# Kernel tuning notes

Measured on AMD Instinct MI355X. Metric: run time of the kernel, lower is better.

Reference implementation:

```python
import jax, jax.numpy as jnp
import numpy as np

B, H, W, C, NH, WS, SS = 32, 56, 56, 192, 6, 7, 3
N = WS * WS
HD = C // NH
NW = (H // WS) * (W // WS)
HID = 4 * C
RPB_SIZE = (2 * WS - 1) * (2 * WS - 1)


def _rel_index():
    coords = np.stack(np.meshgrid(np.arange(WS), np.arange(WS), indexing='ij')).reshape(2, -1)
    rel = (coords[:, :, None] - coords[:, None, :]).transpose(1, 2, 0)
    rel[..., 0] += WS - 1
    rel[..., 1] += WS - 1
    rel[..., 0] *= 2 * WS - 1
    return rel.sum(-1)  # (N, N) int

REL_IDX = jnp.asarray(_rel_index())


def _swin_attn_mask():
    # standard Swin shifted-window mask: -100 for cross-region pairs
    img = np.zeros((H, W))
    cnt = 0
    for hs in (slice(0, -WS), slice(-WS, -SS), slice(-SS, None)):
        for ws_ in (slice(0, -WS), slice(-WS, -SS), slice(-SS, None)):
            img[hs, ws_] = cnt
            cnt += 1
    win = img.reshape(H // WS, WS, W // WS, WS).transpose(0, 2, 1, 3).reshape(-1, N)
    diff = win[:, None, :] - win[:, :, None]
    return np.where(diff != 0, -100.0, 0.0).astype(np.float32)  # (NW, N, N)


def _ln(t, g, b, eps=1e-5):
    mu = t.mean(-1, keepdims=True)
    v = ((t - mu) ** 2).mean(-1, keepdims=True)
    return (t - mu) * jax.lax.rsqrt(v + eps) * g + b


def setup_inputs() -> dict:
    key = jax.random.key(0)
    ks = jax.random.split(key, 12)
    s = 0.02
    return {
        'x': jax.random.normal(ks[0], (B, H * W, C), jnp.float32),
        'attn_mask': jnp.asarray(_swin_attn_mask()),
        'ln1_g': jnp.ones((C,), jnp.float32),
        'ln1_b': jnp.zeros((C,), jnp.float32),
        'qkv_w': jax.random.normal(ks[1], (C, 3 * C), jnp.float32) * s,
        'qkv_b': jnp.zeros((3 * C,), jnp.float32),
        'rpb': jax.random.normal(ks[2], (RPB_SIZE, NH), jnp.float32) * s,
        'proj_w': jax.random.normal(ks[3], (C, C), jnp.float32) * s,
        'proj_b': jnp.zeros((C,), jnp.float32),
        'ln2_g': jnp.ones((C,), jnp.float32),
        'ln2_b': jnp.zeros((C,), jnp.float32),
        'fc1_w': jax.random.normal(ks[4], (C, HID), jnp.float32) * s,
        'fc1_b': jnp.zeros((HID,), jnp.float32),
        'fc2_w': jax.random.normal(ks[5], (HID, C), jnp.float32) * s,
        'fc2_b': jnp.zeros((C,), jnp.float32),
    }


def reference(x, attn_mask, ln1_g, ln1_b, qkv_w, qkv_b, rpb, proj_w, proj_b,
              ln2_g, ln2_b, fc1_w, fc1_b, fc2_w, fc2_b):
    shortcut = x
    h = _ln(x, ln1_g, ln1_b).reshape(B, H, W, C)
    # cyclic shift
    h = jnp.roll(h, (-SS, -SS), axis=(1, 2))
    # window partition -> (B*NW, N, C)
    h = h.reshape(B, H // WS, WS, W // WS, WS, C).transpose(0, 1, 3, 2, 4, 5).reshape(B * NW, N, C)
    qkv = (h @ qkv_w + qkv_b).reshape(B * NW, N, 3, NH, HD).transpose(2, 0, 3, 1, 4)
    q, k, v = qkv[0] * (HD ** -0.5), qkv[1], qkv[2]
    attn = jnp.einsum('bhnd,bhmd->bhnm', q, k)  # (B*NW, NH, N, N)
    bias = rpb[REL_IDX].transpose(2, 0, 1)      # (NH, N, N)
    attn = attn + bias[None]
    attn = attn.reshape(B, NW, NH, N, N) + attn_mask[None, :, None]
    attn = jax.nn.softmax(attn.reshape(B * NW, NH, N, N), axis=-1)
    o = jnp.einsum('bhnm,bhmd->bhnd', attn, v).transpose(0, 2, 1, 3).reshape(B * NW, N, C)
    o = o @ proj_w + proj_b
    # window reverse + reverse shift
    o = o.reshape(B, H // WS, W // WS, WS, WS, C).transpose(0, 1, 3, 2, 4, 5).reshape(B, H, W, C)
    o = jnp.roll(o, (SS, SS), axis=(1, 2)).reshape(B, H * W, C)
    x1 = shortcut + o
    m = _ln(x1, ln2_g, ln2_b)
    m = jax.nn.gelu(m @ fc1_w + fc1_b, approximate=False) @ fc2_w + fc2_b
    return x1 + m
```

## Files before the change

kernel.cpp:

```cpp
#include <hip/hip_runtime.h>
#include <hip/hip_bf16.h>

typedef __hip_bfloat16 bf16;
typedef __attribute__((ext_vector_type(8))) short short8;
typedef __attribute__((ext_vector_type(4))) float f32x4;
typedef __attribute__((ext_vector_type(4))) unsigned short ushort4_t;

#define TOK 100352
#define NWIN 2048
#define CC 192
#define NHEAD 6
#define NT 49

__device__ __forceinline__ float bf2f(bf16 v) { return __bfloat162float(v); }
__device__ __forceinline__ bf16 f2bf(float v) { return __float2bfloat16(v); }
__device__ __forceinline__ float b2f_bits(unsigned short u) {
    return __uint_as_float(((unsigned)u) << 16);
}

__device__ __forceinline__ float ldin(const void* p, size_t i, int f) {
    return f ? ((const float*)p)[i] : bf2f(((const bf16*)p)[i]);
}
__device__ __forceinline__ void stc(bf16* p, float v) { *p = f2bf(v); }
__device__ __forceinline__ void stc(float* p, float v) { *p = v; }
__device__ __forceinline__ float ldc(const bf16* p) { return bf2f(*p); }
__device__ __forceinline__ float ldc(const float* p) { return *p; }

__device__ __forceinline__ float gelu_f(float v) {
    float z = v * 0.70710678118654752f;
    float az = fabsf(z);
    float t = __builtin_amdgcn_rcpf(1.0f + 0.3275911f * az);
    float p = t * (0.254829592f + t * (-0.284496736f + t * (1.421413741f
            + t * (-1.453152027f + t * 1.061405429f))));
    float e = __expf(-az * az);
    float er = copysignf(1.0f - p * e, z);
    return 0.5f * v * (1.0f + er);
}

__device__ __forceinline__ void gl_lds16(const bf16* g, bf16* l) {
    __builtin_amdgcn_global_load_lds(
        (const __attribute__((address_space(1))) unsigned int*)g,
        (__attribute__((address_space(3))) unsigned int*)l, 16, 0, 0);
}

__global__ void dtype_probe_kernel(const void* xraw, int* flag) {
    const unsigned short* u = (const unsigned short*)xraw;
    int lane = threadIdx.x & 63;
    int weird = 0;
    for (int i = lane; i < 4096; i += 64) {
        unsigned int bits = ((unsigned int)u[2 * i]) << 16;
        float v = __uint_as_float(bits);
        if (!(fabsf(v) <= 1e10f)) weird++;
    }
    #pragma unroll
    for (int off = 32; off > 0; off >>= 1) weird += __shfl_xor(weird, off, 64);
    if (lane == 0) *flag = (weird > 256) ? 1 : 0;
}

__global__ void transpose_kernel(const void* __restrict__ in, bf16* __restrict__ out,
                                 int K, int N, const int* __restrict__ flag) {
    int f = *flag;
    int idx = blockIdx.x * 256 + threadIdx.x;
    if (idx >= K * N) return;
    int nn = idx / K, kk = idx % K;
    out[idx] = f2bf(ldin(in, (size_t)kk * N + nn, f));
}

__global__ __launch_bounds__(256) void comb_kernel(
    const void* __restrict__ rpb, const void* __restrict__ mask,
    bf16* __restrict__ comb, const int* __restrict__ flag) {
    int f = *flag;
    int idx = blockIdx.x * 256 + threadIdx.x;
    int m = idx & 63;
    int n = (idx >> 6) & 63;
    int hw = idx >> 12;
    int head = hw % NHEAD, wi = hw / NHEAD;
    float v;
    if (n < NT && m < NT) {
        int nr = n / 7, nc = n % 7, mr = m / 7, mc = m % 7;
        int ridx = (nr - mr + 6) * 13 + (nc - mc + 6);
        v = ldin(rpb, (size_t)ridx * NHEAD + head, f)
          + ldin(mask, (size_t)wi * NT * NT + n * NT + m, f);
    } else {
        v = -1e30f;
    }
    comb[idx] = f2bf(v);
}

__global__ __launch_bounds__(256) void ln1_window_kernel(
    const void* __restrict__ x, const void* __restrict__ g, const void* __restrict__ b,
    bf16* __restrict__ hwin, const int* __restrict__ flag) {
    int f = *flag;
    int wave = threadIdx.x >> 6, lane = threadIdx.x & 63;
    int t = blockIdx.x * 4 + wave;
    int bidx = t / (64 * NT);
    int r = t % (64 * NT);
    int wi = r / NT, n = r % NT;
    int wr = wi >> 3, wc = wi & 7;
    int nr = n / 7, nc = n % 7;
    int si = wr * 7 + nr, sj = wc * 7 + nc;
    int oi = si + 3; if (oi >= 56) oi -= 56;
    int oj = sj + 3; if (oj >= 56) oj -= 56;
    size_t src = ((size_t)bidx * 3136 + oi * 56 + oj) * CC;
    float v0 = ldin(x, src + lane, f);
    float v1 = ldin(x, src + lane + 64, f);
    float v2 = ldin(x, src + lane + 128, f);
    float s = v0 + v1 + v2;
    float sq = v0 * v0 + v1 * v1 + v2 * v2;
    #pragma unroll
    for (int off = 32; off > 0; off >>= 1) {
        s  += __shfl_xor(s, off, 64);
        sq += __shfl_xor(sq, off, 64);
    }
    float mu = s * (1.f / 192.f);
    float var = fmaxf(sq * (1.f / 192.f) - mu * mu, 0.f);
    float rs = rsqrtf(var + 1e-5f);
    bf16* dst = hwin + (size_t)t * CC;
    dst[lane]       = f2bf((v0 - mu) * rs * ldin(g, lane, f)       + ldin(b, lane, f));
    dst[lane + 64]  = f2bf((v1 - mu) * rs * ldin(g, lane + 64, f)  + ldin(b, lane + 64, f));
    dst[lane + 128] = f2bf((v2 - mu) * rs * ldin(g, lane + 128, f) + ldin(b, lane + 128, f));
}

template <int EPI, typename CT>
__global__ __launch_bounds__(256, 4) void gemm_kernel(
    const bf16* __restrict__ A, const bf16* __restrict__ Wt,
    const void* __restrict__ bias, CT* __restrict__ C,
    const CT* __restrict__ resid, int M, int K, int Nc, const int* __restrict__ flag) {
    int f = *flag;
    __shared__ __align__(16) bf16 sb[3][6144];
    int tid = threadIdx.x;
    int wave = tid >> 6, lane = tid & 63;
    int quad = lane >> 4, l16 = lane & 15;

    int nwg = gridDim.x * gridDim.y;
    int bid = blockIdx.y * gridDim.x + blockIdx.x;
    int swz = bid;
    if ((nwg & 7) == 0) {
        int cpx = nwg >> 3;
        swz = (bid & 7) * cpx + (bid >> 3);
    }
    int bn = swz % gridDim.x, bm = swz / gridDim.x;

    const bf16* ag[2];
    #pragma unroll
    for (int j = 0; j < 2; j++)
        ag[j] = A + (size_t)(bm * 128 + (wave * 2 + j) * 16 + (lane >> 2)) * K + (lane & 3) * 8;
    const bf16* bg = Wt + (size_t)(bn * 64 + wave * 16 + (lane >> 2)) * K + (lane & 3) * 8;

    auto STAGE = [&](int t, int buf) {
        gl_lds16(ag[0] + (size_t)t * 32, &sb[buf][(wave * 2 + 0) * 512]);
        gl_lds16(ag[1] + (size_t)t * 32, &sb[buf][(wave * 2 + 1) * 512]);
        gl_lds16(bg    + (size_t)t * 32, &sb[buf][4096 + wave * 512]);
    };

    f32x4 acc[2][4];
    #pragma unroll
    for (int i = 0; i < 2; i++)
        #pragma unroll
        for (int j = 0; j < 4; j++)
            acc[i][j][0] = acc[i][j][1] = acc[i][j][2] = acc[i][j][3] = 0.f;

    const int nt = K >> 5;

    STAGE(0, 0);
    STAGE(1, 1);
    asm volatile("s_waitcnt vmcnt(3)" ::: "memory");
    __builtin_amdgcn_s_barrier();

    int cur = 0;
    for (int t = 0; t < nt; t++) {
        if (t + 2 < nt) {
            int stg = cur + 2; if (stg >= 3) stg -= 3;
            STAGE(t + 2, stg);
        }
        const bf16* sA = &sb[cur][0];
        const bf16* sB = &sb[cur][4096];
        short8 av[2], bv[4];
        #pragma unroll
        for (int tm = 0; tm < 2; tm++)
            av[tm] = *(const short8*)(&sA[(wave * 32 + tm * 16 + l16) * 32 + quad * 8]);
        #pragma unroll
        for (int tn = 0; tn < 4; tn++)
            bv[tn] = *(const short8*)(&sB[(tn * 16 + l16) * 32 + quad * 8]);
        #pragma unroll
        for (int tm = 0; tm < 2; tm++)
            #pragma unroll
            for (int tn = 0; tn < 4; tn++)
                acc[tm][tn] = __builtin_amdgcn_mfma_f32_16x16x32_bf16(av[tm], bv[tn], acc[tm][tn], 0, 0, 0);
        if (t + 1 < nt) {
            if (t + 2 < nt)
                asm volatile("s_waitcnt vmcnt(3) lgkmcnt(0)" ::: "memory");
            else
                asm volatile("s_waitcnt vmcnt(0) lgkmcnt(0)" ::: "memory");
            __builtin_amdgcn_s_barrier();
        }
        cur++; if (cur >= 3) cur -= 3;
    }

    #pragma unroll
    for (int tm = 0; tm < 2; tm++)
        #pragma unroll
        for (int tn = 0; tn < 4; tn++) {
            int col = bn * 64 + tn * 16 + l16;
            float bvs = ldin(bias, col, f);
            #pragma unroll
            for (int r = 0; r < 4; r++) {
                int row = bm * 128 + wave * 32 + tm * 16 + quad * 4 + r;
                float v = acc[tm][tn][r] + bvs;
                if (EPI == 1) v = gelu_f(v);
                if (EPI == 2) v += ldc(&resid[(size_t)row * Nc + col]);
                stc(&C[(size_t)row * Nc + col], v);
            }
        }
}

__global__ __launch_bounds__(256) void attn_mfma_kernel(
    const bf16* __restrict__ qkv, const bf16* __restrict__ comb,
    bf16* __restrict__ attn_out, int wbase) {
    __shared__ __align__(16) bf16 Qs[64 * 40];
    __shared__ __align__(16) bf16 Ks[64 * 40];
    __shared__ __align__(16) bf16 Vt[32 * 72];
    __shared__ __align__(16) bf16 P[64 * 72];

    int head = blockIdx.x % NHEAD;
    int wl = blockIdx.x / NHEAD;
    int wg = wbase + wl;
    int wi = wg & 63;
    int t0 = wl * NT;
    int tg = wg * NT;
    int tid = threadIdx.x;
    int wave = tid >> 6, lane = tid & 63;
    int quad = lane >> 4, l16 = lane & 15;

    {
        int row = tid >> 2;
        int dc = (tid & 3) * 8;
        uint4 qv = make_uint4(0, 0, 0, 0), kv = qv, vv = qv;
        if (row < NT) {
            const bf16* base = qkv + (size_t)(t0 + row) * 576 + head * 32 + dc;
            qv = *(const uint4*)(base);
            kv = *(const uint4*)(base + 192);
            vv = *(const uint4*)(base + 384);
        }
        *(uint4*)(&Qs[row * 40 + dc]) = qv;
        *(uint4*)(&Ks[row * 40 + dc]) = kv;
        bf16 tv[8];
        *(uint4*)tv = vv;
        #pragma unroll
        for (int r = 0; r < 8; r++)
            Vt[(dc + r) * 72 + row] = tv[r];
    }
    __syncthreads();

    const float scale = 0.17677669529663687f;
    int tm = wave;
    int q = tm * 16 + l16;
    const bf16* crow = comb + (((size_t)wi * NHEAD + head) * 64 + q) * 64;

    float s[4][4];
    short8 bfrag = *(const short8*)(&Qs[q * 40 + quad * 8]);
    f32x4 z; z[0] = z[1] = z[2] = z[3] = 0.f;
    #pragma unroll
    for (int tn = 0; tn < 4; tn++) {
        short8 afrag = *(const short8*)(&Ks[(tn * 16 + l16) * 40 + quad * 8]);
        f32x4 acc = __builtin_amdgcn_mfma_f32_16x16x32_bf16(afrag, bfrag, z, 0, 0, 0);
        ushort4_t cb = *(const ushort4_t*)(crow + tn * 16 + quad * 4);
        s[tn][0] = acc[0] * scale + b2f_bits(cb[0]);
        s[tn][1] = acc[1] * scale + b2f_bits(cb[1]);
        s[tn][2] = acc[2] * scale + b2f_bits(cb[2]);
        s[tn][3] = acc[3] * scale + b2f_bits(cb[3]);
    }

    float mx = s[0][0];
    #pragma unroll
    for (int tn = 0; tn < 4; tn++)
        #pragma unroll
        for (int r = 0; r < 4; r++) mx = fmaxf(mx, s[tn][r]);
    mx = fmaxf(mx, __shfl_xor(mx, 16, 64));
    mx = fmaxf(mx, __shfl_xor(mx, 32, 64));
    float sm = 0.f;
    #pragma unroll
    for (int tn = 0; tn < 4; tn++)
        #pragma unroll
        for (int r = 0; r < 4; r++) { s[tn][r] = __expf(s[tn][r] - mx); sm += s[tn][r]; }
    sm += __shfl_xor(sm, 16, 64);
    sm += __shfl_xor(sm, 32, 64);
    float inv = 1.0f / sm;

    #pragma unroll
    for (int tn = 0; tn < 4; tn++) {
        bf16 pk[4];
        #pragma unroll
        for (int r = 0; r < 4; r++) pk[r] = f2bf(s[tn][r] * inv);
        *(uint2*)(&P[q * 72 + tn * 16 + quad * 4]) = *(const uint2*)pk;
    }
    __syncthreads();

    f32x4 oacc[2];
    oacc[0][0] = oacc[0][1] = oacc[0][2] = oacc[0][3] = 0.f;
    oacc[1] = oacc[0];
    #pragma unroll
    for (int kc = 0; kc < 2; kc++) {
        short8 pa = *(const short8*)(&P[(tm * 16 + l16) * 72 + kc * 32 + quad * 8]);
        #pragma unroll
        for (int tn = 0; tn < 2; tn++) {
            short8 vb = *(const short8*)(&Vt[(tn * 16 + l16) * 72 + kc * 32 + quad * 8]);
            oacc[tn] = __builtin_amdgcn_mfma_f32_16x16x32_bf16(pa, vb, oacc[tn], 0, 0, 0);
        }
    }
    #pragma unroll
    for (int tn = 0; tn < 2; tn++) {
        #pragma unroll
        for (int r = 0; r < 4; r++) {
            int n = tm * 16 + quad * 4 + r;
            int d = tn * 16 + l16;
            if (n < NT)
                attn_out[(size_t)(tg + n) * CC + head * 32 + d] = f2bf(oacc[tn][r]);
        }
    }
}

__global__ __launch_bounds__(256) void resid_ln2_kernel(
    const void* __restrict__ x, const bf16* __restrict__ proj,
    const void* __restrict__ g, const void* __restrict__ b,
    float* __restrict__ x1, bf16* __restrict__ h2, const int* __restrict__ flag) {
    int f = *flag;
    int wave = threadIdx.x >> 6, lane = threadIdx.x & 63;
    int tok = blockIdx.x * 4 + wave;
    int bidx = tok / 3136;
    int r = tok % 3136;
    int i = r / 56, j = r % 56;
    int si = i + 53; if (si >= 56) si -= 56;
    int sj = j + 53; if (sj >= 56) sj -= 56;
    int wi = (si / 7) * 8 + sj / 7;
    int n = (si % 7) * 7 + (sj % 7);
    size_t tw = ((size_t)bidx * 64 + wi) * NT + n;
    const bf16* ps = proj + tw * CC;
    size_t xs = (size_t)tok * CC;
    float v0 = ldin(x, xs + lane, f)       + bf2f(ps[lane]);
    float v1 = ldin(x, xs + lane + 64, f)  + bf2f(ps[lane + 64]);
    float v2 = ldin(x, xs + lane + 128, f) + bf2f(ps[lane + 128]);
    float* xd = x1 + (size_t)tok * CC;
    xd[lane] = v0; xd[lane + 64] = v1; xd[lane + 128] = v2;
    float s = v0 + v1 + v2;
    float sq = v0 * v0 + v1 * v1 + v2 * v2;
    #pragma unroll
    for (int off = 32; off > 0; off >>= 1) {
        s  += __shfl_xor(s, off, 64);
        sq += __shfl_xor(sq, off, 64);
    }
    float mu = s * (1.f / 192.f);
    float var = fmaxf(sq * (1.f / 192.f) - mu * mu, 0.f);
    float rs = rsqrtf(var + 1e-5f);
    bf16* dst = h2 + (size_t)tok * CC;
    dst[lane]       = f2bf((v0 - mu) * rs * ldin(g, lane, f)       + ldin(b, lane, f));
    dst[lane + 64]  = f2bf((v1 - mu) * rs * ldin(g, lane + 64, f)  + ldin(b, lane + 64, f));
    dst[lane + 128] = f2bf((v2 - mu) * rs * ldin(g, lane + 128, f) + ldin(b, lane + 128, f));
}

extern "C" void kernel_launch(void* const* d_in, const int* in_sizes, int n_in,
                              void* d_out, int out_size, void* d_ws, size_t ws_size,
                              hipStream_t stream) {
    const void* x        = d_in[0];
    const void* attnmask = d_in[1];
    const void* ln1_g    = d_in[2];
    const void* ln1_b    = d_in[3];
    const void* qkv_w    = d_in[4];
    const void* qkv_b    = d_in[5];
    const void* rpb      = d_in[6];
    const void* proj_w   = d_in[7];
    const void* proj_b   = d_in[8];
    const void* ln2_g    = d_in[9];
    const void* ln2_b    = d_in[10];
    const void* fc1_w    = d_in[11];
    const void* fc1_b    = d_in[12];
    const void* fc2_w    = d_in[13];
    const void* fc2_b    = d_in[14];
    float* out = (float*)d_out;
    char* ws = (char*)d_ws;

    const size_t RSZ = (size_t)TOK * CC * sizeof(bf16);
    const size_t WEXT = 442368 * sizeof(bf16)
                      + (size_t)64 * NHEAD * 64 * 64 * sizeof(bf16)
                      + 64;
    const size_t NEED_BIG = 5 * RSZ + WEXT;

    const int M = TOK;

    if (ws_size >= NEED_BIG) {
        bf16* h_win    = (bf16*)(ws);
        bf16* qkvbuf   = (bf16*)(ws + RSZ);
        bf16* attn_out = (bf16*)(ws + 4 * RSZ);
        bf16* projbuf  = (bf16*)(ws);
        bf16* h2       = (bf16*)(ws + 4 * RSZ);
        bf16* m1buf    = (bf16*)(ws);
        bf16* qkvT     = (bf16*)(ws + 5 * RSZ);
        bf16* projT    = qkvT + 192 * 576;
        bf16* fc1T     = projT + 192 * 192;
        bf16* fc2T     = fc1T + 192 * 768;
        bf16* combT    = fc2T + 768 * 192;
        int*  flag     = (int*)(combT + 64 * NHEAD * 64 * 64);

        dtype_probe_kernel<<<1, 64, 0, stream>>>(x, flag);
        transpose_kernel<<<(192 * 576 + 255) / 256, 256, 0, stream>>>(qkv_w, qkvT, 192, 576, flag);
        transpose_kernel<<<(192 * 192 + 255) / 256, 256, 0, stream>>>(proj_w, projT, 192, 192, flag);
        transpose_kernel<<<(192 * 768 + 255) / 256, 256, 0, stream>>>(fc1_w, fc1T, 192, 768, flag);
        transpose_kernel<<<(768 * 192 + 255) / 256, 256, 0, stream>>>(fc2_w, fc2T, 768, 192, flag);
        comb_kernel<<<(64 * NHEAD * 64 * 64) / 256, 256, 0, stream>>>(rpb, attnmask, combT, flag);

        ln1_window_kernel<<<TOK / 4, 256, 0, stream>>>(x, ln1_g, ln1_b, h_win, flag);

        gemm_kernel<0, bf16><<<dim3(576 / 64, M / 128), 256, 0, stream>>>(
            h_win, qkvT, qkv_b, qkvbuf, (const bf16*)nullptr, M, 192, 576, flag);
        attn_mfma_kernel<<<NWIN * NHEAD, 256, 0, stream>>>(qkvbuf, combT, attn_out, 0);

        gemm_kernel<0, bf16><<<dim3(192 / 64, M / 128), 256, 0, stream>>>(
            attn_out, projT, proj_b, projbuf, (const bf16*)nullptr, M, 192, 192, flag);

        resid_ln2_kernel<<<TOK / 4, 256, 0, stream>>>(x, projbuf, ln2_g, ln2_b, out, h2, flag);

        gemm_kernel<1, bf16><<<dim3(768 / 64, M / 128), 256, 0, stream>>>(
            h2, fc1T, fc1_b, m1buf, (const bf16*)nullptr, M, 192, 768, flag);
        gemm_kernel<2, float><<<dim3(192 / 64, M / 128), 256, 0, stream>>>(
            m1buf, fc2T, fc2_b, out, (const float*)out, M, 768, 192, flag);
    } else {
        bf16* h_win    = (bf16*)(ws);
        bf16* m1buf    = (bf16*)(ws);
        bf16* attn_out = (bf16*)(ws + RSZ);
        bf16* h2       = (bf16*)(ws + RSZ);
        bf16* qkvchunk = (bf16*)(ws + 2 * RSZ);
        bf16* projbuf  = (bf16*)(ws + 2 * RSZ);
        bf16* combT    = (bf16*)(ws + 2 * RSZ + 28901376);
        bf16* qkvT     = (bf16*)(ws + 3 * RSZ);
        bf16* projT    = qkvT + 192 * 576;
        bf16* fc1T     = projT + 192 * 192;
        bf16* fc2T     = fc1T + 192 * 768;
        int*  flag     = (int*)(fc2T + 768 * 192);

        dtype_probe_kernel<<<1, 64, 0, stream>>>(x, flag);
        transpose_kernel<<<(192 * 576 + 255) / 256, 256, 0, stream>>>(qkv_w, qkvT, 192, 576, flag);
        transpose_kernel<<<(192 * 192 + 255) / 256, 256, 0, stream>>>(proj_w, projT, 192, 192, flag);
        transpose_kernel<<<(192 * 768 + 255) / 256, 256, 0, stream>>>(fc1_w, fc1T, 192, 768, flag);
        transpose_kernel<<<(768 * 192 + 255) / 256, 256, 0, stream>>>(fc2_w, fc2T, 768, 192, flag);
        comb_kernel<<<(64 * NHEAD * 64 * 64) / 256, 256, 0, stream>>>(rpb, attnmask, combT, flag);

        ln1_window_kernel<<<TOK / 4, 256, 0, stream>>>(x, ln1_g, ln1_b, h_win, flag);

        const int QCH = 4, QW = NWIN / QCH;
        const int QROWS = QW * NT;
        for (int c = 0; c < QCH; c++) {
            const bf16* a = h_win + (size_t)c * QROWS * CC;
            gemm_kernel<0, bf16><<<dim3(576 / 64, QROWS / 128), 256, 0, stream>>>(
                a, qkvT, qkv_b, qkvchunk, (const bf16*)nullptr, QROWS, 192, 576, flag);
            attn_mfma_kernel<<<QW * NHEAD, 256, 0, stream>>>(
                qkvchunk, combT, attn_out, c * QW);
        }

        gemm_kernel<0, bf16><<<dim3(192 / 64, M / 128), 256, 0, stream>>>(
            attn_out, projT, proj_b, projbuf, (const bf16*)nullptr, M, 192, 192, flag);

        resid_ln2_kernel<<<TOK / 4, 256, 0, stream>>>(x, projbuf, ln2_g, ln2_b, out, h2, flag);

        const int MCH = 4, MR = TOK / MCH;
        for (int c = 0; c < MCH; c++) {
            const bf16* a = h2 + (size_t)c * MR * CC;
            float* oc = out + (size_t)c * MR * CC;
            gemm_kernel<1, bf16><<<dim3(768 / 64, MR / 128), 256, 0, stream>>>(
                a, fc1T, fc1_b, m1buf, (const bf16*)nullptr, MR, 192, 768, flag);
            gemm_kernel<2, float><<<dim3(192 / 64, MR / 128), 256, 0, stream>>>(
                m1buf, fc2T, fc2_b, oc, (const float*)oc, MR, 768, 192, flag);
        }
    }
}
```

Before: 524.7 us.

## Add K=192 GEMM that keeps weight tile in LDS across row blocks

Adds a specialised GEMM for K=192 that loads the whole 64-column weight slice into shared memory once. Each workgroup then streams G blocks of 128 rows of A through a 3-stage buffer, writing out each block's bias (and optional GELU) result before moving on. It is used for the QKV, proj and fc1 GEMMs and is meant to cut repeated weight loads and per-block prologue cost. The trade-off is fewer, longer workgroups with more shared memory each, plus hand-tuned waitcnt counts that must match the load order exactly.

```diff
diff --git a/kernel.cpp b/kernel.cpp
--- a/kernel.cpp
+++ b/kernel.cpp
@@ -119,6 +119,113 @@
     dst[lane]       = f2bf((v0 - mu) * rs * ldin(g, lane, f)       + ldin(b, lane, f));
     dst[lane + 64]  = f2bf((v1 - mu) * rs * ldin(g, lane + 64, f)  + ldin(b, lane + 64, f));
     dst[lane + 128] = f2bf((v2 - mu) * rs * ldin(g, lane + 128, f) + ldin(b, lane + 128, f));
+}
+
+template <int EPI, int G>
+__global__ __launch_bounds__(256) void gemm192_kernel(
+    const bf16* __restrict__ A, const bf16* __restrict__ Wt,
+    const void* __restrict__ bias, bf16* __restrict__ C,
+    int Nc, const int* __restrict__ flag) {
+    const int K = 192;
+    int f = *flag;
+    __shared__ __align__(16) bf16 sbA[3 * 4096];
+    __shared__ __align__(16) bf16 sbB[6 * 2048];
+    int tid = threadIdx.x;
+    int wave = tid >> 6, lane = tid & 63;
+    int quad = lane >> 4, l16 = lane & 15;
+
+    int nwg = gridDim.x * gridDim.y;
+    int bid = blockIdx.y * gridDim.x + blockIdx.x;
+    int swz = bid;
+    if ((nwg & 7) == 0) {
+        int cpx = nwg >> 3;
+        swz = (bid & 7) * cpx + (bid >> 3);
+    }
+    int bn = swz % gridDim.x, bm = swz / gridDim.x;
+
+    const bf16* ag[2];
+    #pragma unroll
+    for (int j = 0; j < 2; j++)
+        ag[j] = A + (size_t)(bm * (128 * G) + (wave * 2 + j) * 16 + (lane >> 2)) * K
+                  + (lane & 3) * 8;
+    const bf16* bg = Wt + (size_t)(bn * 64 + wave * 16 + (lane >> 2)) * K + (lane & 3) * 8;
+
+    #pragma unroll
+    for (int s = 0; s < 6; s++)
+        gl_lds16(bg + s * 32, &sbB[s * 2048 + wave * 512]);
+    #pragma unroll
+    for (int j = 0; j < 2; j++) {
+        gl_lds16(ag[j],      &sbA[0 * 4096 + (wave * 2 + j) * 512]);
+        gl_lds16(ag[j] + 32, &sbA[1 * 4096 + (wave * 2 + j) * 512]);
+    }
+    asm volatile("s_waitcnt vmcnt(2)" ::: "memory");
+    __builtin_amdgcn_s_barrier();
+
+    float bvs4[4];
+    #pragma unroll
+    for (int tn = 0; tn < 4; tn++)
+        bvs4[tn] = ldin(bias, bn * 64 + tn * 16 + l16, f);
+
+    f32x4 acc[2][4];
+    #pragma unroll
+    for (int i = 0; i < 2; i++)
+        #pragma unroll
+        for (int j = 0; j < 4; j++)
+            acc[i][j][0] = acc[i][j][1] = acc[i][j][2] = acc[i][j][3] = 0.f;
+
+    const int total = 6 * G;
+    #pragma unroll
+    for (int t = 0; t < total; t++) {
+        if (t + 2 < total) {
+            int tt = t + 2;
+            int rb2 = tt / 6, kk2 = tt - rb2 * 6;
+            size_t off = (size_t)rb2 * (128 * K) + kk2 * 32;
+            int buf2 = tt % 3;
+            gl_lds16(ag[0] + off, &sbA[buf2 * 4096 + (wave * 2 + 0) * 512]);
+            gl_lds16(ag[1] + off, &sbA[buf2 * 4096 + (wave * 2 + 1) * 512]);
+        }
+        int kk = t % 6, buf = t % 3;
+        const bf16* sA = &sbA[buf * 4096];
+        const bf16* sB = &sbB[kk * 2048];
+        short8 av[2], bv[4];
+        #pragma unroll
+        for (int tm = 0; tm < 2; tm++)
+            av[tm] = *(const short8*)(&sA[(wave * 32 + tm * 16 + l16) * 32 + quad * 8]);
+        #pragma unroll
+        for (int tn = 0; tn < 4; tn++)
+            bv[tn] = *(const short8*)(&sB[(tn * 16 + l16) * 32 + quad * 8]);
+        #pragma unroll
+        for (int tm = 0; tm < 2; tm++)
+            #pragma unroll
+            for (int tn = 0; tn < 4; tn++)
+                acc[tm][tn] = __builtin_amdgcn_mfma_f32_16x16x32_bf16(av[tm], bv[tn], acc[tm][tn], 0, 0, 0);
+        if (kk == 5) {
+            int rb = t / 6;
+            #pragma unroll
+            for (int tm = 0; tm < 2; tm++)
+                #pragma unroll
+                for (int tn = 0; tn < 4; tn++) {
+                    int col = bn * 64 + tn * 16 + l16;
+                    #pragma unroll
+                    for (int r = 0; r < 4; r++) {
+                        int row = bm * (128 * G) + rb * 128 + wave * 32 + tm * 16 + quad * 4 + r;
+                        float v = acc[tm][tn][r] + bvs4[tn];
+                        if (EPI == 1) v = gelu_f(v);
+                        C[(size_t)row * Nc + col] = f2bf(v);
+                        acc[tm][tn][r] = 0.f;
+                    }
+                }
+        }
+        if (t + 1 < total) {
+            if (t + 2 >= total)
+                asm volatile("s_waitcnt vmcnt(0) lgkmcnt(0)" ::: "memory");
+            else if ((kk == 5 || kk == 0) && t >= 5)
+                asm volatile("s_waitcnt vmcnt(34) lgkmcnt(0)" ::: "memory");
+            else
+                asm volatile("s_waitcnt vmcnt(2) lgkmcnt(0)" ::: "memory");
+            __builtin_amdgcn_s_barrier();
+        }
+    }
 }
 
 template <int EPI, typename CT>
@@ -410,17 +517,17 @@
 
         ln1_window_kernel<<<TOK / 4, 256, 0, stream>>>(x, ln1_g, ln1_b, h_win, flag);
 
-        gemm_kernel<0, bf16><<<dim3(576 / 64, M / 128), 256, 0, stream>>>(
-            h_win, qkvT, qkv_b, qkvbuf, (const bf16*)nullptr, M, 192, 576, flag);
+        gemm192_kernel<0, 4><<<dim3(576 / 64, M / 512), 256, 0, stream>>>(
+            h_win, qkvT, qkv_b, qkvbuf, 576, flag);
         attn_mfma_kernel<<<NWIN * NHEAD, 256, 0, stream>>>(qkvbuf, combT, attn_out, 0);
 
-        gemm_kernel<0, bf16><<<dim3(192 / 64, M / 128), 256, 0, stream>>>(
-            attn_out, projT, proj_b, projbuf, (const bf16*)nullptr, M, 192, 192, flag);
+        gemm192_kernel<0, 2><<<dim3(192 / 64, M / 256), 256, 0, stream>>>(
+            attn_out, projT, proj_b, projbuf, 192, flag);
 
         resid_ln2_kernel<<<TOK / 4, 256, 0, stream>>>(x, projbuf, ln2_g, ln2_b, out, h2, flag);
 
-        gemm_kernel<1, bf16><<<dim3(768 / 64, M / 128), 256, 0, stream>>>(
-            h2, fc1T, fc1_b, m1buf, (const bf16*)nullptr, M, 192, 768, flag);
+        gemm192_kernel<1, 4><<<dim3(768 / 64, M / 512), 256, 0, stream>>>(
+            h2, fc1T, fc1_b, m1buf, 768, flag);
         gemm_kernel<2, float><<<dim3(192 / 64, M / 128), 256, 0, stream>>>(
             m1buf, fc2T, fc2_b, out, (const float*)out, M, 768, 192, flag);
     } else {
@@ -450,14 +557,14 @@
         const int QROWS = QW * NT;
         for (int c = 0; c < QCH; c++) {
             const bf16* a = h_win + (size_t)c * QROWS * CC;
-            gemm_kernel<0, bf16><<<dim3(576 / 64, QROWS / 128), 256, 0, stream>>>(
-                a, qkvT, qkv_b, qkvchunk, (const bf16*)nullptr, QROWS, 192, 576, flag);
+            gemm192_kernel<0, 4><<<dim3(576 / 64, QROWS / 512), 256, 0, stream>>>(
+                a, qkvT, qkv_b, qkvchunk, 576, flag);
             attn_mfma_kernel<<<QW * NHEAD, 256, 0, stream>>>(
                 qkvchunk, combT, attn_out, c * QW);
         }
 
-        gemm_kernel<0, bf16><<<dim3(192 / 64, M / 128), 256, 0, stream>>>(
-            attn_out, projT, proj_b, projbuf, (const bf16*)nullptr, M, 192, 192, flag);
+        gemm192_kernel<0, 2><<<dim3(192 / 64, M / 256), 256, 0, stream>>>(
+            attn_out, projT, proj_b, projbuf, 192, flag);
 
         resid_ln2_kernel<<<TOK / 4, 256, 0, stream>>>(x, projbuf, ln2_g, ln2_b, out, h2, flag);
 
@@ -465,8 +572,8 @@
         for (int c = 0; c < MCH; c++) {
             const bf16* a = h2 + (size_t)c * MR * CC;
             float* oc = out + (size_t)c * MR * CC;
-            gemm_kernel<1, bf16><<<dim3(768 / 64, MR / 128), 256, 0, stream>>>(
-                a, fc1T, fc1_b, m1buf, (const bf16*)nullptr, MR, 192, 768, flag);
+            gemm192_kernel<1, 4><<<dim3(768 / 64, MR / 512), 256, 0, stream>>>(
+                a, fc1T, fc1_b, m1buf, 768, flag);
             gemm_kernel<2, float><<<dim3(192 / 64, MR / 128), 256, 0, stream>>>(
                 m1buf, fc2T, fc2_b, oc, (const float*)oc, MR, 768, 192, flag);
         }
```

Measured after the change: 548.7 us. 4.6% more time.
